# Optimization experiments

Measured on AMD Instinct MI355X. Metric: run time of the kernel, lower is better.

## Reference

```python
import jax, jax.numpy as jnp
import numpy as np
import math

NUM_LAYERS = 2
NUM_HEADS = 8
D_MODEL = 256
D_FF = 4 * D_MODEL
FACTOR = 5
B, L, F_IN = 8, 2048, 32


def layer_norm(x, g, b, eps=1e-5):
    m = x.mean(-1, keepdims=True)
    v = ((x - m) ** 2).mean(-1, keepdims=True)
    return (x - m) * jax.lax.rsqrt(v + eps) * g + b


def prob_attention(q, k, v, idx):
    # q,k,v: [B,H,L,Dh]; idx: [L,S] sampled key indices per query (ProbSparse)
    Bq, H, Lq, Dh = q.shape
    u = min(FACTOR * math.ceil(math.log(Lq)), Lq)  # number of 'active' queries
    k_s = k[:, :, idx, :]                              # [B,H,L,S,Dh] gathered keys
    qk_s = jnp.einsum('bhld,bhlsd->bhls', q, k_s)      # sampled scores
    M = qk_s.max(-1) - qk_s.sum(-1) / Lq               # sparsity measure [B,H,L]
    _, top = jax.lax.top_k(M, u)                       # [B,H,u] active query idx
    q_red = jnp.take_along_axis(q, top[..., None], axis=2)   # [B,H,u,Dh]
    scores = jnp.einsum('bhud,bhld->bhul', q_red, k) * (1.0 / math.sqrt(Dh))
    attn = jax.nn.softmax(scores, axis=-1)             # [B,H,u,L]
    upd = jnp.einsum('bhul,bhld->bhud', attn, v)       # [B,H,u,Dh]
    # initial context = mean of V (mask_flag=False), then scatter active rows
    ctx = jnp.broadcast_to(v.mean(2, keepdims=True), (Bq, H, Lq, Dh))
    bi = jnp.arange(Bq)[:, None, None]
    hi = jnp.arange(H)[None, :, None]
    return ctx.at[bi, hi, top].set(upd)


def setup_inputs() -> dict:
    key = jax.random.key(0)
    ks = jax.random.split(key, 16)
    S = min(FACTOR * math.ceil(math.log(L)), L)  # 40
    std = 0.02

    def w(k, shape):
        return jax.random.normal(k, shape, jnp.float32) * std

    inp = {}
    inp['x'] = jax.random.normal(ks[0], (B, L, F_IN), jnp.float32)
    inp['idx_sample'] = jax.random.randint(ks[1], (NUM_LAYERS, L, S), 0, L)
    inp['w_in'] = w(ks[2], (F_IN, D_MODEL)); inp['b_in'] = jnp.zeros((D_MODEL,), jnp.float32)
    inp['wq'] = w(ks[3], (NUM_LAYERS, D_MODEL, D_MODEL)); inp['bq'] = jnp.zeros((NUM_LAYERS, D_MODEL), jnp.float32)
    inp['wk'] = w(ks[4], (NUM_LAYERS, D_MODEL, D_MODEL)); inp['bk'] = jnp.zeros((NUM_LAYERS, D_MODEL), jnp.float32)
    inp['wv'] = w(ks[5], (NUM_LAYERS, D_MODEL, D_MODEL)); inp['bv'] = jnp.zeros((NUM_LAYERS, D_MODEL), jnp.float32)
    inp['wo'] = w(ks[6], (NUM_LAYERS, D_MODEL, D_MODEL)); inp['bo'] = jnp.zeros((NUM_LAYERS, D_MODEL), jnp.float32)
    inp['w_ff1'] = w(ks[7], (NUM_LAYERS, D_MODEL, D_FF)); inp['b_ff1'] = jnp.zeros((NUM_LAYERS, D_FF), jnp.float32)
    inp['w_ff2'] = w(ks[8], (NUM_LAYERS, D_FF, D_MODEL)); inp['b_ff2'] = jnp.zeros((NUM_LAYERS, D_MODEL), jnp.float32)
    inp['ln1_g'] = jnp.ones((NUM_LAYERS, D_MODEL), jnp.float32); inp['ln1_b'] = jnp.zeros((NUM_LAYERS, D_MODEL), jnp.float32)
    inp['ln2_g'] = jnp.ones((NUM_LAYERS, D_MODEL), jnp.float32); inp['ln2_b'] = jnp.zeros((NUM_LAYERS, D_MODEL), jnp.float32)
    inp['w_fc1'] = w(ks[9], (D_MODEL, 64)); inp['b_fc1'] = jnp.zeros((64,), jnp.float32)
    inp['w_fc2'] = w(ks[10], (64, 1)); inp['b_fc2'] = jnp.zeros((1,), jnp.float32)
    return inp


def reference(x, idx_sample, w_in, b_in, wq, bq, wk, bk, wv, bv, wo, bo,
              w_ff1, b_ff1, w_ff2, b_ff2, ln1_g, ln1_b, ln2_g, ln2_b,
              w_fc1, b_fc1, w_fc2, b_fc2):
    Bx, Lx, _ = x.shape
    h = x @ w_in + b_in  # [B,L,D_MODEL]
    for i in range(NUM_LAYERS):
        q = (h @ wq[i] + bq[i]).reshape(Bx, Lx, NUM_HEADS, -1).transpose(0, 2, 1, 3)
        k = (h @ wk[i] + bk[i]).reshape(Bx, Lx, NUM_HEADS, -1).transpose(0, 2, 1, 3)
        v = (h @ wv[i] + bv[i]).reshape(Bx, Lx, NUM_HEADS, -1).transpose(0, 2, 1, 3)
        ctx = prob_attention(q, k, v, idx_sample[i])            # [B,H,L,Dh]
        ctx = ctx.transpose(0, 2, 1, 3).reshape(Bx, Lx, D_MODEL)
        new_x = ctx @ wo[i] + bo[i]
        h = layer_norm(h + new_x, ln1_g[i], ln1_b[i])
        y = jax.nn.relu(h @ w_ff1[i] + b_ff1[i]) @ w_ff2[i] + b_ff2[i]
        h = layer_norm(h + y, ln2_g[i], ln2_b[i])
    last = h[:, -1, :]                      # take final time step
    out = jax.nn.relu(last @ w_fc1 + b_fc1) @ w_fc2 + b_fc2
    return out[:, None, :]                  # unsqueeze(1) -> [B,1,output_size]
```

## Files before the change

### kernel.cpp

```cpp
#include <hip/hip_runtime.h>
#include <math.h>

#define BB 8
#define LL 2048
#define DM 256
#define NH 8
#define DH 32
#define DFF 1024
#define SS 40
#define UU 40
#define BL (BB*LL)
#define NSL 8

#define SCP 260
#define KP  40
#define VP  34

typedef unsigned short ushort_t;
typedef unsigned char uchar_t;
typedef __attribute__((ext_vector_type(8))) short short8;
typedef __attribute__((ext_vector_type(4))) float f32x4;

__device__ inline ushort_t f2b(float f)
{
    unsigned int u = __float_as_uint(f);
    u += 0x7fff + ((u >> 16) & 1);
    return (ushort_t)(u >> 16);
}

__device__ inline float blo(unsigned int u) { return __uint_as_float(u << 16); }
__device__ inline float bhi(unsigned int u) { return __uint_as_float(u & 0xffff0000u); }

__device__ inline void gload16(const void* g, const void* l)
{
    __builtin_amdgcn_global_load_lds(
        (const __attribute__((address_space(1))) unsigned int*)g,
        (__attribute__((address_space(3))) unsigned int*)l, 16, 0, 0);
}

template<int RELU, int OUT_MODE>
__global__ __launch_bounds__(256)
void gemm_mfma(const ushort_t* __restrict__ A, const ushort_t* __restrict__ Bt,
               const float* __restrict__ bias, void* __restrict__ Cout,
               void* __restrict__ aux, int M, int N, int K)
{
    __shared__ ushort_t Asl[128 * 32];
    __shared__ ushort_t Bsl[128 * 32];

    const int t    = threadIdx.x;
    const int lane = t & 63;
    const int wv   = t >> 6;
    const int row0 = blockIdx.x * 128;
    const int col0 = blockIdx.y * 128;
    const int wr   = (wv >> 1) * 64;
    const int wc   = (wv & 1) * 64;
    const int quad = lane >> 4;
    const int l16  = lane & 15;

    f32x4 acc[4][4];
    #pragma unroll
    for (int i = 0; i < 4; ++i)
        #pragma unroll
        for (int j = 0; j < 4; ++j)
            acc[i][j] = 0.f;

    for (int k0 = 0; k0 < K; k0 += 32) {
        __syncthreads();
        #pragma unroll
        for (int r = 0; r < 2; ++r) {
            int g = r * 256 + t;
            const ushort_t* ga = A  + (size_t)(row0 + (g >> 2)) * K + k0 + (g & 3) * 8;
            const ushort_t* gb = Bt + (size_t)(col0 + (g >> 2)) * K + k0 + (g & 3) * 8;
            int lbase = (r * 256 + wv * 64) * 16;
            gload16(ga, (const char*)Asl + lbase);
            gload16(gb, (const char*)Bsl + lbase);
        }
        __syncthreads();

        short8 af[4], bfr[4];
        #pragma unroll
        for (int mi = 0; mi < 4; ++mi)
            af[mi] = *(const short8*)&Asl[(wr + mi * 16 + l16) * 32 + quad * 8];
        #pragma unroll
        for (int ni = 0; ni < 4; ++ni)
            bfr[ni] = *(const short8*)&Bsl[(wc + ni * 16 + l16) * 32 + quad * 8];
        #pragma unroll
        for (int mi = 0; mi < 4; ++mi)
            #pragma unroll
            for (int ni = 0; ni < 4; ++ni)
                acc[mi][ni] = __builtin_amdgcn_mfma_f32_16x16x32_bf16(
                    af[mi], bfr[ni], acc[mi][ni], 0, 0, 0);
    }

    #pragma unroll
    for (int mi = 0; mi < 4; ++mi) {
        #pragma unroll
        for (int ni = 0; ni < 4; ++ni) {
            int col = col0 + wc + ni * 16 + l16;
            float bb = bias[col];
            #pragma unroll
            for (int r = 0; r < 4; ++r) {
                int row = row0 + wr + mi * 16 + quad * 4 + r;
                float v = acc[mi][ni][r] + bb;
                if (RELU) v = v > 0.f ? v : 0.f;
                if (OUT_MODE == 0) {
                    ((float*)Cout)[(size_t)row * N + col] = v;
                } else if (OUT_MODE == 1) {
                    int tensor = col >> 8;
                    int c2 = col & 255;
                    int b  = row >> 11, l = row & (LL - 1);
                    int hh = c2 >> 5,  dh = c2 & 31;
                    int bh = b * NH + hh;
                    size_t bi = (((size_t)bh * LL + l) << 5) + dh;
                    ushort_t vb16 = f2b(v);
                    ((ushort_t*)Cout)[(size_t)tensor * (BB*NH*LL*DH) + bi] = vb16;
                    if (tensor == 1)
                        ((ushort_t*)aux)[(((size_t)l << 6) + bh) * 32 + dh] = vb16;
                } else if (OUT_MODE == 2) {
                    ((ushort_t*)Cout)[(size_t)row * N + col] = f2b(v);
                } else {
                    ((float*)Cout)[(size_t)row * N + col] = v;
                    ((ushort_t*)aux)[(size_t)row * N + col] = f2b(v);
                }
            }
        }
    }
}

template<int HEAD>
__global__ __launch_bounds__(256)
void gemmln_k(const ushort_t* __restrict__ A, const ushort_t* __restrict__ Bt,
              const float* __restrict__ bias, float* __restrict__ h,
              ushort_t* __restrict__ hb, const float* __restrict__ g,
              const float* __restrict__ beta, int K,
              const float* __restrict__ w1, const float* __restrict__ b1,
              const float* __restrict__ w2, const float* __restrict__ b2,
              float* __restrict__ out)
{
    __shared__ ushort_t Asl[32 * 32];
    __shared__ ushort_t Bsl[256 * 32];
    __shared__ float rs[4][32], rs2[4][32];
    __shared__ float hrowS[256];

    const int t    = threadIdx.x;
    const int lane = t & 63;
    const int wv   = t >> 6;
    const int row0 = blockIdx.x * 32;
    const int wc   = wv * 64;
    const int quad = lane >> 4;
    const int l16  = lane & 15;

    f32x4 acc[2][4];
    #pragma unroll
    for (int i = 0; i < 2; ++i)
        #pragma unroll
        for (int j = 0; j < 4; ++j)
            acc[i][j] = 0.f;

    for (int k0 = 0; k0 < K; k0 += 32) {
        __syncthreads();
        if (wv < 2) {
            const ushort_t* ga = A + (size_t)(row0 + (t >> 2)) * K + k0 + (t & 3) * 8;
            gload16(ga, (const char*)Asl + wv * 1024);
        }
        #pragma unroll
        for (int r = 0; r < 4; ++r) {
            int gg = r * 256 + t;
            const ushort_t* gb = Bt + (size_t)(gg >> 2) * K + k0 + (gg & 3) * 8;
            gload16(gb, (const char*)Bsl + (r * 256 + wv * 64) * 16);
        }
        __syncthreads();

        short8 af[2], bfr[4];
        #pragma unroll
        for (int mi = 0; mi < 2; ++mi)
            af[mi] = *(const short8*)&Asl[(mi * 16 + l16) * 32 + quad * 8];
        #pragma unroll
        for (int ni = 0; ni < 4; ++ni)
            bfr[ni] = *(const short8*)&Bsl[(wc + ni * 16 + l16) * 32 + quad * 8];
        #pragma unroll
        for (int mi = 0; mi < 2; ++mi)
            #pragma unroll
            for (int ni = 0; ni < 4; ++ni)
                acc[mi][ni] = __builtin_amdgcn_mfma_f32_16x16x32_bf16(
                    af[mi], bfr[ni], acc[mi][ni], 0, 0, 0);
    }

    float gcol[4], bcol[4];
    #pragma unroll
    for (int ni = 0; ni < 4; ++ni) {
        int col = wc + ni * 16 + l16;
        gcol[ni] = g[col];
        bcol[ni] = beta[col];
    }
    float ps[2][4], ps2[2][4];
    #pragma unroll
    for (int mi = 0; mi < 2; ++mi) {
        #pragma unroll
        for (int r = 0; r < 4; ++r) {
            int row = row0 + mi * 16 + quad * 4 + r;
            float s = 0.f, s2 = 0.f;
            #pragma unroll
            for (int ni = 0; ni < 4; ++ni) {
                int col = wc + ni * 16 + l16;
                float v = acc[mi][ni][r] + bias[col] + h[(size_t)row * DM + col];
                acc[mi][ni][r] = v;
                s += v;
                s2 += v * v;
            }
            ps[mi][r] = s;
            ps2[mi][r] = s2;
        }
    }
    #pragma unroll
    for (int off = 1; off < 16; off <<= 1) {
        #pragma unroll
        for (int mi = 0; mi < 2; ++mi)
            #pragma unroll
            for (int r = 0; r < 4; ++r) {
                ps[mi][r]  += __shfl_xor(ps[mi][r],  off, 16);
                ps2[mi][r] += __shfl_xor(ps2[mi][r], off, 16);
            }
    }
    if (l16 == 0) {
        #pragma unroll
        for (int mi = 0; mi < 2; ++mi)
            #pragma unroll
            for (int r = 0; r < 4; ++r) {
                int lrow = mi * 16 + quad * 4 + r;
                rs[wv][lrow]  = ps[mi][r];
                rs2[wv][lrow] = ps2[mi][r];
            }
    }
    __syncthreads();

    #pragma unroll
    for (int mi = 0; mi < 2; ++mi) {
        #pragma unroll
        for (int r = 0; r < 4; ++r) {
            int lrow = mi * 16 + quad * 4 + r;
            int row  = row0 + lrow;
            float tot  = rs[0][lrow] + rs[1][lrow] + rs[2][lrow] + rs[3][lrow];
            float tot2 = rs2[0][lrow] + rs2[1][lrow] + rs2[2][lrow] + rs2[3][lrow];
            float mean = tot * (1.f / (float)DM);
            float var  = tot2 * (1.f / (float)DM) - mean * mean;
            float inv  = 1.0f / sqrtf(var + 1e-5f);
            #pragma unroll
            for (int ni = 0; ni < 4; ++ni) {
                int col = wc + ni * 16 + l16;
                float val = (acc[mi][ni][r] - mean) * inv * gcol[ni] + bcol[ni];
                h[(size_t)row * DM + col]  = val;
                hb[(size_t)row * DM + col] = f2b(val);
                if (HEAD && lrow == 31) hrowS[col] = val;
            }
        }
    }

    if (HEAD) {
        __syncthreads();
        if ((blockIdx.x & 63) == 63 && t < 64) {
            int b = blockIdx.x >> 6;
            float s = 0.f;
            for (int kk = 0; kk < DM; ++kk)
                s = fmaf(hrowS[kk], w1[kk * 64 + t], s);
            s += b1[t];
            s = s > 0.f ? s : 0.f;
            float contrib = s * w2[t];
            #pragma unroll
            for (int off = 32; off > 0; off >>= 1)
                contrib += __shfl_down(contrib, off, 64);
            if (t == 0) out[b] = contrib + b2[0];
        }
    }
}

__device__ inline void tcvt_dev(float (*tile)[33], const float* __restrict__ src,
                                ushort_t* __restrict__ dst, int K, int N,
                                int matStride, int bi)
{
    int tilesN = N >> 5;
    int tpm = (K >> 5) * tilesN;
    int m   = bi / tpm;
    int tid = bi % tpm;
    int k0 = (tid / tilesN) << 5, n0 = (tid % tilesN) << 5;
    const float* s = src + (size_t)m * K * N;
    ushort_t*    d = dst + (size_t)m * matStride;
    int r = threadIdx.x >> 5, c = threadIdx.x & 31;
    #pragma unroll
    for (int i = 0; i < 4; ++i)
        tile[r + 8 * i][c] = s[(size_t)(k0 + r + 8 * i) * N + n0 + c];
    __syncthreads();
    #pragma unroll
    for (int i = 0; i < 4; ++i)
        d[(size_t)(n0 + r + 8 * i) * K + k0 + c] = f2b(tile[c][r + 8 * i]);
}

__global__ __launch_bounds__(256)
void preproc_k(const float* __restrict__ wq, const float* __restrict__ wk,
               const float* __restrict__ wv, const float* __restrict__ wo,
               const float* __restrict__ wf1, const float* __restrict__ wf2,
               const float* __restrict__ w_in,
               const float* __restrict__ bq, const float* __restrict__ bk,
               const float* __restrict__ bv, const float* __restrict__ x,
               ushort_t* __restrict__ wqkvT, ushort_t* __restrict__ woT,
               ushort_t* __restrict__ wf1T, ushort_t* __restrict__ wf2T,
               ushort_t* __restrict__ w_inT, float* __restrict__ bqkv,
               ushort_t* __restrict__ xb16)
{
    __shared__ float tile[32][33];
    int b = blockIdx.x;
    if (b < 512) {
        int which = b >> 7, lb = b & 127;
        const float* src = which == 0 ? wq : which == 1 ? wk : which == 2 ? wv : wo;
        ushort_t* dst = which == 0 ? wqkvT : which == 1 ? wqkvT + 65536
                       : which == 2 ? wqkvT + 131072 : woT;
        int stride = which == 3 ? 65536 : 768 * 256;
        tcvt_dev(tile, src, dst, DM, DM, stride, lb);
    } else if (b < 1024) {
        tcvt_dev(tile, wf1, wf1T, DM, DFF, 1024 * 256, b - 512);
    } else if (b < 1536) {
        tcvt_dev(tile, wf2, wf2T, DFF, DM, 256 * 1024, b - 1024);
    } else if (b < 1544) {
        tcvt_dev(tile, w_in, w_inT, 32, DM, 256 * 32, b - 1536);
    } else if (b < 1550) {
        int t = (b - 1544) * 256 + threadIdx.x;
        int i = t / 768, j = t % 768;
        const float* s = j < 256 ? bq : (j < 512 ? bk : bv);
        bqkv[t] = s[i * 256 + (j & 255)];
    } else {
        int tid = (b - 1550) * 256 + threadIdx.x;
        float4 v = ((const float4*)x)[tid];
        unsigned int lo = f2b(v.x) | ((unsigned int)f2b(v.y) << 16);
        unsigned int hi = f2b(v.z) | ((unsigned int)f2b(v.w) << 16);
        ((uint2*)xb16)[tid] = make_uint2(lo, hi);
    }
}

__global__ __launch_bounds__(256)
void metric2_k(const ushort_t* __restrict__ qb16, const ushort_t* __restrict__ kT,
               const int* __restrict__ idx, float* __restrict__ Mout,
               unsigned int* __restrict__ jidx32)
{
    __shared__ float mst[64][5];
    int t = threadIdx.x;
    int w = t >> 6, lane = t & 63;
    int l = blockIdx.x * 4 + w;

    if (t < 64) {
        int zb = t >> 3, sel = t & 7;
        int zl = blockIdx.x * 4 + (sel >> 1), half = sel & 1;
        jidx32[(size_t)(zb * LL + zl) * 2 + half] = 0;
    }

    float4 q[8];
    {
        const uint4* qr4 = (const uint4*)(qb16 + ((size_t)(lane * LL + l) << 5));
        #pragma unroll
        for (int i = 0; i < 4; ++i) {
            uint4 u = qr4[i];
            q[2 * i]     = make_float4(blo(u.x), bhi(u.x), blo(u.y), bhi(u.y));
            q[2 * i + 1] = make_float4(blo(u.z), bhi(u.z), blo(u.w), bhi(u.w));
        }
    }

    int r40 = idx[l * SS + (lane < SS ? lane : SS - 1)];

    float mx = -3e38f, sm = 0.f;
    for (int s = 0; s < SS; ++s) {
        int r = __shfl(r40, s, 64);
        const uint4* kr = (const uint4*)(kT + (((size_t)r << 6) + lane) * 32);
        float d = 0.f;
        #pragma unroll
        for (int ww = 0; ww < 4; ++ww) {
            uint4 kv = kr[ww];
            float4 qa = q[2 * ww], qb2 = q[2 * ww + 1];
            d = fmaf(blo(kv.x), qa.x, d);
            d = fmaf(bhi(kv.x), qa.y, d);
            d = fmaf(blo(kv.y), qa.z, d);
            d = fmaf(bhi(kv.y), qa.w, d);
            d = fmaf(blo(kv.z), qb2.x, d);
            d = fmaf(bhi(kv.z), qb2.y, d);
            d = fmaf(blo(kv.w), qb2.z, d);
            d = fmaf(bhi(kv.w), qb2.w, d);
        }
        mx = fmaxf(mx, d);
        sm += d;
    }
    mst[lane][w] = mx - sm * (1.0f / (float)LL);
    __syncthreads();

    int bh = t >> 2, ls = t & 3;
    Mout[(size_t)bh * LL + blockIdx.x * 4 + ls] = mst[bh][ls];
}

__global__ __launch_bounds__(512)
void topkf_k(const float* __restrict__ Mout, int* __restrict__ top,
             uchar_t* __restrict__ jidx)
{
    __shared__ float cvS[320];
    __shared__ int   ciS[320];
    int bh = blockIdx.x;
    int t  = threadIdx.x;
    int lane = t & 63, w = t >> 6;
    int l0 = w << 8;

    float v[4];
    #pragma unroll
    for (int i = 0; i < 4; ++i)
        v[i] = Mout[(size_t)bh * LL + l0 + i * 64 + lane];

    for (int r = 0; r < UU; ++r) {
        float bv = -3e38f; int bi = 1 << 30;
        #pragma unroll
        for (int i = 0; i < 4; ++i) {
            int idx = l0 + i * 64 + lane;
            if (v[i] > bv || (v[i] == bv && idx < bi)) { bv = v[i]; bi = idx; }
        }
        #pragma unroll
        for (int off = 32; off > 0; off >>= 1) {
            float ov = __shfl_down(bv, off, 64);
            int   oi = __shfl_down(bi, off, 64);
            if (ov > bv || (ov == bv && oi < bi)) { bv = ov; bi = oi; }
        }
        bv = __shfl(bv, 0, 64);
        bi = __shfl(bi, 0, 64);
        if (lane == 0) { cvS[w * UU + r] = bv; ciS[w * UU + r] = bi; }
        int rel = bi - l0;
        if ((rel & 63) == lane) v[rel >> 6] = -3e38f;
    }
    __syncthreads();

    for (int c = t; c < 320; c += 512) {
        float mv = cvS[c]; int mi = ciS[c];
        int rank = 0;
        for (int j = 0; j < 320; ++j)
            rank += (cvS[j] > mv) || (cvS[j] == mv && ciS[j] < mi);
        if (rank < UU) {
            top[bh * UU + rank] = mi;
            int b = bh >> 3, hh = bh & 7;
            jidx[(size_t)(b * LL + mi) * 8 + hh] = (uchar_t)(rank + 1);
        }
    }
}

__global__ __launch_bounds__(256)
void attnupd_k(const ushort_t* __restrict__ qb16, const ushort_t* __restrict__ kb16,
               const ushort_t* __restrict__ vb16, const int* __restrict__ top,
               float* __restrict__ mP, float* __restrict__ sP,
               float* __restrict__ OP, float* __restrict__ vmeanP)
{
    __shared__ ushort_t qs[48 * KP];
    __shared__ ushort_t kv[256 * KP];
    __shared__ float    sc[48 * SCP];
    __shared__ float    msh[UU];
    __shared__ float    red[8][32];

    int blk = blockIdx.x;
    int sl  = blk & (NSL - 1);
    int bh  = blk >> 3;
    int t   = threadIdx.x;
    int l0  = sl << 8;
    int lane = t & 63, wvx = t >> 6;
    int quad = lane >> 4, l16 = lane & 15;
    const float scale = 0.17677669529663687f;

    for (int i = t; i < 48 * 32; i += 256) {
        int j = i >> 5, dd = i & 31;
        qs[(i >> 5) * KP + dd] = (j < UU)
            ? qb16[((size_t)(bh * LL + top[bh * UU + j]) << 5) + dd] : (ushort_t)0;
    }
    {
        const unsigned int* krow =
            (const unsigned int*)(kb16 + ((size_t)(bh * LL + l0 + t) << 5));
        #pragma unroll
        for (int i = 0; i < 16; ++i)
            ((unsigned int*)kv)[t * (KP / 2) + i] = krow[i];
    }
    __syncthreads();

    {
        short8 afq[3];
        #pragma unroll
        for (int mt = 0; mt < 3; ++mt)
            afq[mt] = *(const short8*)&qs[(mt * 16 + l16) * KP + quad * 8];
        #pragma unroll
        for (int n4 = 0; n4 < 4; ++n4) {
            int nt = wvx * 4 + n4;
            short8 bk = *(const short8*)&kv[(nt * 16 + l16) * KP + quad * 8];
            #pragma unroll
            for (int mt = 0; mt < 3; ++mt) {
                f32x4 dd = {0.f, 0.f, 0.f, 0.f};
                dd = __builtin_amdgcn_mfma_f32_16x16x32_bf16(afq[mt], bk, dd, 0, 0, 0);
                #pragma unroll
                for (int r = 0; r < 4; ++r)
                    sc[(mt * 16 + quad * 4 + r) * SCP + nt * 16 + l16] = dd[r] * scale;
            }
        }
    }
    __syncthreads();

    int j8 = t >> 5, d = t & 31;
    #pragma unroll
    for (int g = 0; g < 5; ++g) {
        int j = g * 8 + j8;
        float4 a = *(const float4*)&sc[j * SCP + 4 * d];
        float4 b = *(const float4*)&sc[j * SCP + 128 + 4 * d];
        float m = fmaxf(fmaxf(fmaxf(a.x, a.y), fmaxf(a.z, a.w)),
                        fmaxf(fmaxf(b.x, b.y), fmaxf(b.z, b.w)));
        #pragma unroll
        for (int off = 16; off > 0; off >>= 1)
            m = fmaxf(m, __shfl_down(m, off, 64));
        if (d == 0) msh[j] = m;
    }
    __syncthreads();

    #pragma unroll 2
    for (int i = t; i < UU * 64; i += 256) {
        int j = i >> 6;
        float* p = &sc[j * SCP + (i & 63) * 4];
        float4 e = *(float4*)p;
        float mm = msh[j];
        e.x = __expf(e.x - mm); e.y = __expf(e.y - mm);
        e.z = __expf(e.z - mm); e.w = __expf(e.w - mm);
        *(float4*)p = e;
    }
    __syncthreads();

    int pq = bh * NSL + sl;

    #pragma unroll
    for (int g = 0; g < 5; ++g) {
        int j = g * 8 + j8;
        float4 a = *(const float4*)&sc[j * SCP + 4 * d];
        float4 b = *(const float4*)&sc[j * SCP + 128 + 4 * d];
        float s = a.x + a.y + a.z + a.w + b.x + b.y + b.z + b.w;
        #pragma unroll
        for (int off = 16; off > 0; off >>= 1)
            s += __shfl_down(s, off, 64);
        if (d == 0) { sP[pq * UU + j] = s; mP[pq * UU + j] = msh[j]; }
    }
    {
        const unsigned int* vrow =
            (const unsigned int*)(vb16 + ((size_t)(bh * LL + l0 + t) << 5));
        #pragma unroll
        for (int i = 0; i < 16; ++i)
            *(unsigned int*)&kv[t * VP + 2 * i] = vrow[i];
        const ushort_t* base = vb16 + ((size_t)(bh * LL + l0 + j8 * 32) << 5) + d;
        float s = 0.f;
        #pragma unroll 8
        for (int i = 0; i < 32; ++i)
            s += __uint_as_float((unsigned int)base[(size_t)i << 5] << 16);
        red[j8][d] = s;
    }
    __syncthreads();

    if (t < 32) {
        float tot = 0.f;
        #pragma unroll
        for (int p = 0; p < 8; ++p) tot += red[p][t];
        vmeanP[pq * 32 + t] = tot;
    }

    if (wvx < 3) {
        f32x4 acc0 = {0.f, 0.f, 0.f, 0.f};
        f32x4 acc1 = {0.f, 0.f, 0.f, 0.f};
        #pragma unroll
        for (int ks = 0; ks < 8; ++ks) {
            float4 p0 = *(const float4*)&sc[(wvx * 16 + l16) * SCP + ks * 32 + quad * 8];
            float4 p1 = *(const float4*)&sc[(wvx * 16 + l16) * SCP + ks * 32 + quad * 8 + 4];
            short8 af;
            af[0] = (short)f2b(p0.x); af[1] = (short)f2b(p0.y);
            af[2] = (short)f2b(p0.z); af[3] = (short)f2b(p0.w);
            af[4] = (short)f2b(p1.x); af[5] = (short)f2b(p1.y);
            af[6] = (short)f2b(p1.z); af[7] = (short)f2b(p1.w);
            #pragma unroll
            for (int nt = 0; nt < 2; ++nt) {
                short8 bf;
                #pragma unroll
                for (int jj = 0; jj < 8; ++jj)
                    bf[jj] = (short)kv[(ks * 32 + quad * 8 + jj) * VP + nt * 16 + l16];
                if (nt == 0)
                    acc0 = __builtin_amdgcn_mfma_f32_16x16x32_bf16(af, bf, acc0, 0, 0, 0);
                else
                    acc1 = __builtin_amdgcn_mfma_f32_16x16x32_bf16(af, bf, acc1, 0, 0, 0);
            }
        }
        #pragma unroll
        for (int r = 0; r < 4; ++r) {
            int j = wvx * 16 + quad * 4 + r;
            if (j < UU) {
                OP[((size_t)pq * UU + j) * 32 + l16]      = acc0[r];
                OP[((size_t)pq * UU + j) * 32 + 16 + l16] = acc1[r];
            }
        }
    }
}

__global__ __launch_bounds__(256)
void fillcomb_k(const float* __restrict__ vmeanP, const uchar_t* __restrict__ jidx,
                const float* __restrict__ mP, const float* __restrict__ sP,
                const float* __restrict__ OP, ushort_t* __restrict__ ctxb)
{
    int tid = blockIdx.x * 256 + threadIdx.x;
    int pr   = tid & 127;
    int rowi = tid >> 7;
    int b    = rowi >> 11;
    int hh   = pr >> 4;
    int bh   = b * 8 + hh;
    int d0   = (pr * 2) & 31;
    int j    = (int)jidx[(size_t)rowi * 8 + hh];

    float v0, v1;
    if (j == 0) {
        float s0 = 0.f, s1 = 0.f;
        #pragma unroll
        for (int q = 0; q < NSL; ++q) {
            s0 += vmeanP[(bh * NSL + q) * 32 + d0];
            s1 += vmeanP[(bh * NSL + q) * 32 + d0 + 1];
        }
        v0 = s0 * (1.f / (float)LL);
        v1 = s1 * (1.f / (float)LL);
    } else {
        int jj = j - 1;
        float M = -3e38f;
        #pragma unroll
        for (int q = 0; q < NSL; ++q) M = fmaxf(M, mP[(bh * NSL + q) * UU + jj]);
        float S = 0.f, O0 = 0.f, O1 = 0.f;
        #pragma unroll
        for (int q = 0; q < NSL; ++q) {
            float wgt = __expf(mP[(bh * NSL + q) * UU + jj] - M);
            S  = fmaf(sP[(bh * NSL + q) * UU + jj], wgt, S);
            O0 = fmaf(OP[((size_t)(bh * NSL + q) * UU + jj) * 32 + d0], wgt, O0);
            O1 = fmaf(OP[((size_t)(bh * NSL + q) * UU + jj) * 32 + d0 + 1], wgt, O1);
        }
        v0 = O0 / S;
        v1 = O1 / S;
    }
    ((unsigned int*)ctxb)[tid] = (unsigned int)f2b(v0) | ((unsigned int)f2b(v1) << 16);
}

extern "C" void kernel_launch(void* const* d_in, const int* in_sizes, int n_in,
                              void* d_out, int out_size, void* d_ws, size_t ws_size,
                              hipStream_t stream)
{
    const float* x    = (const float*)d_in[0];
    const int*   idx  = (const int*)  d_in[1];
    const float* w_in = (const float*)d_in[2];
    const float* b_in = (const float*)d_in[3];
    const float* wq   = (const float*)d_in[4];
    const float* bq   = (const float*)d_in[5];
    const float* wk   = (const float*)d_in[6];
    const float* bk   = (const float*)d_in[7];
    const float* wv   = (const float*)d_in[8];
    const float* bv   = (const float*)d_in[9];
    const float* wo   = (const float*)d_in[10];
    const float* bo   = (const float*)d_in[11];
    const float* wf1  = (const float*)d_in[12];
    const float* bf1  = (const float*)d_in[13];
    const float* wf2  = (const float*)d_in[14];
    const float* bf2  = (const float*)d_in[15];
    const float* g1   = (const float*)d_in[16];
    const float* be1  = (const float*)d_in[17];
    const float* g2   = (const float*)d_in[18];
    const float* be2  = (const float*)d_in[19];
    const float* wfc1 = (const float*)d_in[20];
    const float* bfc1 = (const float*)d_in[21];
    const float* wfc2 = (const float*)d_in[22];
    const float* bfc2 = (const float*)d_in[23];
    float* out = (float*)d_out;

    float* ws = (float*)d_ws;
    float*    h     = ws;
    ushort_t* q16   = (ushort_t*)(ws + 4194304);
    ushort_t* k16   = q16 + 4194304;
    ushort_t* v16   = q16 + 8388608;
    ushort_t* ctxb  = q16;
    ushort_t* ffbb  = (ushort_t*)(ws + 6291456);
    float*    attnS = ws + 16777216;
    ushort_t* kT16  = (ushort_t*)attnS;
    float*    Mbuf  = attnS + 2097152;
    float*    vmeP  = attnS + 2269184;
    float*    OP    = attnS + 2285568;
    float*    mP    = attnS + 2940928;
    float*    sP    = attnS + 2961408;
    uchar_t*  jidx  = (uchar_t*)(attnS + 2981888);
    float*    scr   = ws + 20971520;
    ushort_t* xb16  = (ushort_t*)scr;
    int*      top   = (int*)(scr + 264192);
    ushort_t* hb    = (ushort_t*)(scr + 266752);
    ushort_t* wqkvT = (ushort_t*)(scr + 2363904);
    ushort_t* woT   = (ushort_t*)(scr + 2560512);
    ushort_t* wf1T  = (ushort_t*)(scr + 2626048);
    ushort_t* wf2T  = (ushort_t*)(scr + 2888192);
    ushort_t* w_inT = (ushort_t*)(scr + 3150336);
    float*    bqkv  = scr + 3154432;

    dim3 blk(256);

    preproc_k<<<dim3(2062), blk, 0, stream>>>(
        wq, wk, wv, wo, wf1, wf2, w_in, bq, bk, bv, x,
        wqkvT, woT, wf1T, wf2T, w_inT, bqkv, xb16);

    gemm_mfma<0,3><<<dim3(BL/128, 2), blk, 0, stream>>>(
        xb16, w_inT, b_in, (void*)h, (void*)hb, BL, DM, 32);

    for (int i = 0; i < 2; ++i) {
        gemm_mfma<0,1><<<dim3(BL/128, 6), blk, 0, stream>>>(
            hb, wqkvT + (size_t)i*768*256, bqkv + i*768, (void*)q16, (void*)kT16,
            BL, 768, DM);

        metric2_k<<<dim3(512), blk, 0, stream>>>(
            q16, kT16, idx + (size_t)i*LL*SS, Mbuf, (unsigned int*)jidx);
        topkf_k<<<dim3(BB*NH), dim3(512), 0, stream>>>(Mbuf, top, jidx);
        attnupd_k<<<dim3(BB*NH*NSL), blk, 0, stream>>>(q16, k16, v16, top, mP, sP, OP, vmeP);
        fillcomb_k<<<dim3(BL*DM/512), blk, 0, stream>>>(vmeP, jidx, mP, sP, OP, ctxb);

        gemmln_k<0><<<dim3(BL/32), blk, 0, stream>>>(
            ctxb, woT + (size_t)i*256*256, bo + i*DM, h, hb,
            g1 + i*DM, be1 + i*DM, DM,
            nullptr, nullptr, nullptr, nullptr, nullptr);

        gemm_mfma<1,2><<<dim3(BL/128, 8), blk, 0, stream>>>(
            hb, wf1T + (size_t)i*1024*256, bf1 + i*DFF, (void*)ffbb, nullptr, BL, DFF, DM);

        if (i == 1) {
            gemmln_k<1><<<dim3(BL/32), blk, 0, stream>>>(
                ffbb, wf2T + (size_t)i*256*1024, bf2 + i*DM, h, hb,
                g2 + i*DM, be2 + i*DM, DFF,
                wfc1, bfc1, wfc2, bfc2, out);
        } else {
            gemmln_k<0><<<dim3(BL/32), blk, 0, stream>>>(
                ffbb, wf2T + (size_t)i*256*1024, bf2 + i*DM, h, hb,
                g2 + i*DM, be2 + i*DM, DFF,
                nullptr, nullptr, nullptr, nullptr, nullptr);
        }
    }
}
```

Baseline: 469.0 us.

## Double-buffer gemmln LDS tiles with BK=64, XOR swizzle, and early residual loads

Rewrites the GEMM+LayerNorm kernel main loop to use double-buffered shared memory with a K step of 64, issuing global loads for the next stage before computing the current one. Explicit vmcnt waits replace the paired syncthreads. The LDS layout uses an XOR swizzle to reduce bank conflicts. Residual h and bias values are loaded before the loop so their latency overlaps the GEMM. In exchange, LDS use roughly quadruples, which may lower occupancy, and the hand-tuned waitcnt depends on the exact number of outstanding loads.

```diff
diff --git a/kernel.cpp b/kernel.cpp
--- a/kernel.cpp
+++ b/kernel.cpp
@@ -137,8 +137,8 @@
               const float* __restrict__ w2, const float* __restrict__ b2,
               float* __restrict__ out)
 {
-    __shared__ ushort_t Asl[32 * 32];
-    __shared__ ushort_t Bsl[256 * 32];
+    __shared__ ushort_t Asl[2][32 * 64];
+    __shared__ ushort_t Bsl[2][256 * 64];
     __shared__ float rs[4][32], rs2[4][32];
     __shared__ float hrowS[256];
 
@@ -150,60 +150,102 @@
     const int quad = lane >> 4;
     const int l16  = lane & 15;
 
-    f32x4 acc[2][4];
-    #pragma unroll
-    for (int i = 0; i < 2; ++i)
-        #pragma unroll
-        for (int j = 0; j < 4; ++j)
-            acc[i][j] = 0.f;
-
-    for (int k0 = 0; k0 < K; k0 += 32) {
-        __syncthreads();
-        if (wv < 2) {
-            const ushort_t* ga = A + (size_t)(row0 + (t >> 2)) * K + k0 + (t & 3) * 8;
-            gload16(ga, (const char*)Asl + wv * 1024);
-        }
-        #pragma unroll
-        for (int r = 0; r < 4; ++r) {
-            int gg = r * 256 + t;
-            const ushort_t* gb = Bt + (size_t)(gg >> 2) * K + k0 + (gg & 3) * 8;
-            gload16(gb, (const char*)Bsl + (r * 256 + wv * 64) * 16);
-        }
-        __syncthreads();
-
-        short8 af[2], bfr[4];
-        #pragma unroll
-        for (int mi = 0; mi < 2; ++mi)
-            af[mi] = *(const short8*)&Asl[(mi * 16 + l16) * 32 + quad * 8];
-        #pragma unroll
-        for (int ni = 0; ni < 4; ++ni)
-            bfr[ni] = *(const short8*)&Bsl[(wc + ni * 16 + l16) * 32 + quad * 8];
-        #pragma unroll
-        for (int mi = 0; mi < 2; ++mi)
-            #pragma unroll
-            for (int ni = 0; ni < 4; ++ni)
-                acc[mi][ni] = __builtin_amdgcn_mfma_f32_16x16x32_bf16(
-                    af[mi], bfr[ni], acc[mi][ni], 0, 0, 0);
-    }
-
-    float gcol[4], bcol[4];
+    float gcol[4], bcol[4], bic[4];
+    float hres[2][4][4];
     #pragma unroll
     for (int ni = 0; ni < 4; ++ni) {
         int col = wc + ni * 16 + l16;
         gcol[ni] = g[col];
         bcol[ni] = beta[col];
-    }
-    float ps[2][4], ps2[2][4];
-    #pragma unroll
-    for (int mi = 0; mi < 2; ++mi) {
+        bic[ni]  = bias[col];
+    }
+    #pragma unroll
+    for (int mi = 0; mi < 2; ++mi)
         #pragma unroll
         for (int r = 0; r < 4; ++r) {
             int row = row0 + mi * 16 + quad * 4 + r;
+            #pragma unroll
+            for (int ni = 0; ni < 4; ++ni)
+                hres[mi][r][ni] = h[(size_t)row * DM + wc + ni * 16 + l16];
+        }
+
+    f32x4 acc[2][4];
+    #pragma unroll
+    for (int i = 0; i < 2; ++i)
+        #pragma unroll
+        for (int j = 0; j < 4; ++j)
+            acc[i][j] = 0.f;
+
+    auto stage = [&](int bf, int k0) {
+        {
+            int row = t >> 3, c8 = t & 7;
+            const ushort_t* ga =
+                A + (size_t)(row0 + row) * K + k0 + ((c8 ^ (row & 7)) * 8);
+            gload16(ga, (const char*)&Asl[bf][0] + (wv * 64) * 16);
+        }
+        #pragma unroll
+        for (int r = 0; r < 8; ++r) {
+            int gg = r * 256 + t;
+            int row = gg >> 3, c8 = gg & 7;
+            const ushort_t* gb =
+                Bt + (size_t)row * K + k0 + ((c8 ^ (row & 7)) * 8);
+            gload16(gb, (const char*)&Bsl[bf][0] + (r * 256 + wv * 64) * 16);
+        }
+    };
+
+    const int NS = K >> 6;
+    stage(0, 0);
+
+    for (int ks = 0; ks < NS; ++ks) {
+        int cur = ks & 1;
+        if (ks + 1 < NS) {
+            stage(cur ^ 1, (ks + 1) << 6);
+            asm volatile("s_waitcnt vmcnt(9)" ::: "memory");
+        } else {
+            asm volatile("s_waitcnt vmcnt(0)" ::: "memory");
+        }
+        __builtin_amdgcn_sched_barrier(0);
+        __builtin_amdgcn_s_barrier();
+
+        short8 af[2][2], bfr[4][2];
+        #pragma unroll
+        for (int mi = 0; mi < 2; ++mi) {
+            int row = mi * 16 + l16;
+            #pragma unroll
+            for (int kk = 0; kk < 2; ++kk)
+                af[mi][kk] = *(const short8*)
+                    &Asl[cur][row * 64 + (((kk * 4 + quad) ^ (row & 7)) * 8)];
+        }
+        #pragma unroll
+        for (int ni = 0; ni < 4; ++ni) {
+            int row = wc + ni * 16 + l16;
+            #pragma unroll
+            for (int kk = 0; kk < 2; ++kk)
+                bfr[ni][kk] = *(const short8*)
+                    &Bsl[cur][row * 64 + (((kk * 4 + quad) ^ (row & 7)) * 8)];
+        }
+        #pragma unroll
+        for (int kk = 0; kk < 2; ++kk)
+            #pragma unroll
+            for (int mi = 0; mi < 2; ++mi)
+                #pragma unroll
+                for (int ni = 0; ni < 4; ++ni)
+                    acc[mi][ni] = __builtin_amdgcn_mfma_f32_16x16x32_bf16(
+                        af[mi][kk], bfr[ni][kk], acc[mi][ni], 0, 0, 0);
+
+        __builtin_amdgcn_sched_barrier(0);
+        __builtin_amdgcn_s_barrier();
+    }
+
+    float ps[2][4], ps2[2][4];
+    #pragma unroll
+    for (int mi = 0; mi < 2; ++mi) {
+        #pragma unroll
+        for (int r = 0; r < 4; ++r) {
             float s = 0.f, s2 = 0.f;
             #pragma unroll
             for (int ni = 0; ni < 4; ++ni) {
-                int col = wc + ni * 16 + l16;
-                float v = acc[mi][ni][r] + bias[col] + h[(size_t)row * DM + col];
+                float v = acc[mi][ni][r] + bic[ni] + hres[mi][r][ni];
                 acc[mi][ni][r] = v;
                 s += v;
                 s2 += v * v;
```

New measurement: 449.2 us. -4.2%, faster.
